# Performance work log

Hardware: AMD Instinct MI355X
Metric: run time of the kernel (lower is better)

The kernel has to match this reference:

```python
import jax, jax.numpy as jnp
import numpy as np
from jax import lax

DN = ('NCHW', 'OIHW', 'NCHW')


def setup_inputs() -> dict:
    key = jax.random.key(0)
    k_x, k0, k1, k2, k3 = jax.random.split(key, 5)
    return {
        'x': jax.random.normal(k_x, (16, 1, 256, 256), dtype=jnp.float32),
        'w0': jax.random.normal(k0, (16, 1, 25, 25), dtype=jnp.float32) * 0.05,
        'w1': jax.random.normal(k1, (16, 1, 49, 49), dtype=jnp.float32) * 0.02,
        'w2': jax.random.normal(k2, (16, 1, 97, 97), dtype=jnp.float32) * 0.01,
        'w3': jax.random.normal(k3, (16, 1, 193, 193), dtype=jnp.float32) * 0.005,
    }


def _energy(x, w, scale):
    # valid conv -> square -> global average pool, divided by scale. [B, 16]
    y = lax.conv_general_dilated(x, w, window_strides=(1, 1), padding='VALID',
                                 dimension_numbers=DN)
    return jnp.mean(y * y, axis=(2, 3)) / scale


def reference(x, w0, w1, w2, w3):
    feats = [
        _energy(x, w0, 1.0),
        _energy(x, w1, 2.0),
        _energy(x, w2, 4.0),
        _energy(x, w3, 8.0),
    ]
    y = jnp.stack(feats, axis=2)  # [B, 16, 4] == cat of squeezed [B,16,1] along dim 2
    y1, y2 = y[:, :8, :], y[:, 8:, :]  # split(8, dim=1)
    return y1 + y2  # [B, 8, 4]
```

## Files before the change

kernel.cpp:

```cpp
#include <hip/hip_runtime.h>
#include <hip/hip_bf16.h>

typedef __attribute__((ext_vector_type(8))) short short8v;
typedef __attribute__((ext_vector_type(4))) float f32x4;

#define IMG 256
#define NIMG 16
#define XB_ELEMS (NIMG * IMG * IMG)

#define WQ0 0u
#define WQ1 102400u
#define WQ2 503808u
#define WQ3 2093056u
#define WQEND 7624704u

#define BUFB 16384

__global__ void xconvert_kernel(const float* __restrict__ x,
                                __hip_bfloat16* __restrict__ xb) {
  int i = blockIdx.x * blockDim.x + threadIdx.x;
  if (i < XB_ELEMS) xb[i] = __float2bfloat16(x[i]);
}

__global__ void wpack_kernel(const float* __restrict__ w,
                             unsigned short* __restrict__ wq,
                             int K, int NSV, int total) {
  for (int idx = blockIdx.x * blockDim.x + threadIdx.x; idx < total;
       idx += gridDim.x * blockDim.x) {
    int e = idx & 7, lane = (idx >> 3) & 63, rest = idx >> 9;
    int sv = rest % NSV; rest /= NSV;
    int u = rest % K, sig = rest / K;
    int o = lane & 15;
    int v = sv * 32 + (lane >> 4) * 8 + e - sig;
    float val = (v >= 0 && v < K) ? w[(o * K + u) * K + v] : 0.0f;
    __hip_bfloat16 h = __float2bfloat16(val);
    wq[idx] = *(unsigned short*)&h;
  }
}

template <int GM, int NSV, int JBA>
__device__ __forceinline__ void kbody(int c, int rb0, int rb1, const char* bufc,
                                      const unsigned short* __restrict__ Wa,
                                      const unsigned short* __restrict__ Wb,
                                      int cbBase, int lr, f32x4 (&acc)[2][2][JBA]) {
#pragma unroll 1
  for (int rbL = rb0; rbL < rb1; ++rbL) {
    const int rowLoc = rbL + lr;
    const char* rbase = bufc + rowLoc * 512;
    const int u0i = 16 * c + rbL;
#pragma unroll
    for (int sv = 0; sv < NSV; ++sv) {
      short8v a_[JBA];
#pragma unroll
      for (int jb = 0; jb < JBA; ++jb) {
        int cb = cbBase + 16 * jb + 64 * sv;
        int addr = (cb & ~127) + ((((cb >> 4) ^ rowLoc) & 7) << 4);
        a_[jb] = *(const short8v*)(rbase + addr);
      }
      if (GM & 1) {
        const int wo = (u0i * NSV + sv) * 512;
        short8v ba = *(const short8v*)(Wa + wo);
        short8v bb = *(const short8v*)(Wb + wo);
#pragma unroll
        for (int jb = 0; jb < JBA; ++jb) {
          acc[0][0][jb] = __builtin_amdgcn_mfma_f32_16x16x32_bf16(a_[jb], ba, acc[0][0][jb], 0, 0, 0);
          acc[0][1][jb] = __builtin_amdgcn_mfma_f32_16x16x32_bf16(a_[jb], bb, acc[0][1][jb], 0, 0, 0);
        }
      }
      if (GM & 2) {
        const int wo = ((u0i - 16) * NSV + sv) * 512;
        short8v ba = *(const short8v*)(Wa + wo);
        short8v bb = *(const short8v*)(Wb + wo);
#pragma unroll
        for (int jb = 0; jb < JBA; ++jb) {
          acc[1][0][jb] = __builtin_amdgcn_mfma_f32_16x16x32_bf16(a_[jb], ba, acc[1][0][jb], 0, 0, 0);
          acc[1][1][jb] = __builtin_amdgcn_mfma_f32_16x16x32_bf16(a_[jb], bb, acc[1][1][jb], 0, 0, 0);
        }
      }
    }
  }
}

template <int KL, int KFULL, int NSV, int JBA, int WC, int HOUT, int SIDX>
__device__ __forceinline__ void conv_scale(const unsigned short* __restrict__ xb,
                                           const unsigned short* __restrict__ wq_s,
                                           float* __restrict__ E, char* lds,
                                           int n, int i0, int u0, int q) {
  constexpr int M16 = KL >> 4, R = KL & 15;
  constexpr int NCH = M16 + (R ? 2 : 1);
  constexpr unsigned SSTRIDE = (unsigned)KFULL * NSV * 512;

  const int wv = threadIdx.x >> 6, lane = threadIdx.x & 63;
  const int lr = lane & 15, lg = lane >> 4;
  const bool isProd = (WC < 8) && (wv >= WC);
  const unsigned short* Xn = xb + ((unsigned)n << 16);
  const int rowG0 = i0 + u0;

  const unsigned short* Wa = wq_s + (unsigned)(2 * q) * SSTRIDE +
                             (unsigned)(u0 * NSV) * 512 + lane * 8;
  const unsigned short* Wb = Wa + SSTRIDE;

  auto stage = [&](int cn) {
    char* dst = lds + (cn & 1) * BUFB;
    constexpr int NSTG = (WC < 8) ? (8 - WC) : 8;
    const int sid = (WC < 8) ? (wv - WC) : wv;
    constexpr int M = (16 + NSTG - 1) / NSTG;
#pragma unroll
    for (int k2 = 0; k2 < M; ++k2) {
      int ib = sid + NSTG * k2;
      if (ib >= 16) ib = 0;
      int P = ib * 1024 + lane * 16;
      int lrow = P >> 9;
      int slot = (P >> 4) & 31;
      int srcslot = (slot & ~7) | ((slot ^ lrow) & 7);
      int grow = rowG0 + cn * 16 + lrow;
      if (grow > 255) grow = 255;
      const unsigned short* gp = Xn + (grow << 8) + srcslot * 8;
      __builtin_amdgcn_global_load_lds(
          (const __attribute__((address_space(1))) unsigned int*)(const void*)gp,
          (__attribute__((address_space(3))) unsigned int*)(void*)(dst + P), 16, 0, 0);
    }
  };

  if (isProd) {
    stage(0);
    asm volatile("s_waitcnt vmcnt(0)" ::: "memory");
    __builtin_amdgcn_s_barrier();
    for (int c = 0; c < NCH; ++c) {
      if (c + 1 < NCH) {
        stage(c + 1);
        asm volatile("s_waitcnt vmcnt(0)" ::: "memory");
      }
      __builtin_amdgcn_s_barrier();
    }
    return;
  }

  f32x4 acc[2][2][JBA];
#pragma unroll
  for (int g = 0; g < 2; ++g)
#pragma unroll
    for (int sj = 0; sj < 2; ++sj)
#pragma unroll
      for (int jb = 0; jb < JBA; ++jb) acc[g][sj][jb] = (f32x4)(0.0f);

  const int t0 = wv * JBA;
  const int cbBase = 16 * t0 + 16 * lg;

  if (WC == 8) {
    stage(0);
    asm volatile("s_waitcnt vmcnt(0)" ::: "memory");
  }
  __builtin_amdgcn_s_barrier();

#define STEP_PRE(c)  if (WC == 8 && (c) + 1 < NCH) stage((c) + 1);
#define STEP_POST()  if (WC == 8) asm volatile("s_waitcnt vmcnt(0)" ::: "memory"); \
                     __builtin_amdgcn_s_barrier();

  {
    const char* bufc = lds;
    STEP_PRE(0)
    kbody<1, NSV, JBA>(0, 0, 16, bufc, Wa, Wb, cbBase, lr, acc);
    STEP_POST()
  }
#pragma unroll 1
  for (int c = 1; c < M16; ++c) {
    const char* bufc = lds + (c & 1) * BUFB;
    STEP_PRE(c)
    kbody<3, NSV, JBA>(c, 0, 16, bufc, Wa, Wb, cbBase, lr, acc);
    STEP_POST()
  }
  if (R > 0) {
    {
      const char* bufc = lds + (M16 & 1) * BUFB;
      STEP_PRE(M16)
      kbody<3, NSV, JBA>(M16, 0, R, bufc, Wa, Wb, cbBase, lr, acc);
      kbody<2, NSV, JBA>(M16, R, 16, bufc, Wa, Wb, cbBase, lr, acc);
      STEP_POST()
    }
    {
      const char* bufc = lds + ((M16 + 1) & 1) * BUFB;
      kbody<2, NSV, JBA>(M16 + 1, 0, R, bufc, Wa, Wb, cbBase, lr, acc);
      STEP_POST()
    }
  } else {
    const char* bufc = lds + (M16 & 1) * BUFB;
    kbody<2, NSV, JBA>(M16, 0, 16, bufc, Wa, Wb, cbBase, lr, acc);
    STEP_POST()
  }
#undef STEP_PRE
#undef STEP_POST

  float esum = 0.0f;
#pragma unroll
  for (int g = 0; g < 2; ++g)
#pragma unroll
    for (int sj = 0; sj < 2; ++sj)
#pragma unroll
      for (int jb = 0; jb < JBA; ++jb) {
        int j = 8 * (t0 + jb) + 2 * q + sj;
#pragma unroll
        for (int r2 = 0; r2 < 4; ++r2) {
          int i = i0 + 16 * g + 4 * lg + r2;
          float v = acc[g][sj][jb][r2];
          esum += (i < HOUT && j < HOUT) ? v * v : 0.0f;
        }
      }
  esum += __shfl_xor(esum, 16, 64);
  esum += __shfl_xor(esum, 32, 64);
  if (lg == 0) atomicAdd(&E[SIDX * 256 + n * 16 + lr], esum);
}

__global__ __launch_bounds__(512, 4) void conv_mfma_kernel(
    const unsigned short* __restrict__ xb, const unsigned short* __restrict__ wq,
    float* __restrict__ E) {
  __shared__ char lds[2 * BUFB];
  int b = blockIdx.x;
  if (b < 256) {
    int q = (b & 7) >> 1;
    int rest = ((b >> 3) << 1) | (b & 1);
    int ks = rest & 1, ig = (rest >> 1) & 1, n = rest >> 2;
    if (ks == 0) conv_scale<96, 193, 7, 2, 4, 64, 3>(xb, wq + WQ3, E, lds, n, ig * 32, 0, q);
    else         conv_scale<97, 193, 7, 2, 4, 64, 3>(xb, wq + WQ3, E, lds, n, ig * 32, 96, q);
  } else if (b < 896) {
    int bl = b - 256;
    int q = (bl & 7) >> 1;
    int rest = ((bl >> 3) << 1) | (bl & 1);
    int ks = rest & 1, r2 = rest >> 1;
    int ig = r2 % 5, n = r2 / 5;
    if (ks == 0) conv_scale<48, 97, 4, 4, 5, 160, 2>(xb, wq + WQ2, E, lds, n, ig * 32, 0, q);
    else         conv_scale<49, 97, 4, 4, 5, 160, 2>(xb, wq + WQ2, E, lds, n, ig * 32, 48, q);
  } else if (b < 1344) {
    int bl = b - 896;
    int q = (bl & 7) >> 1;
    int rest = ((bl >> 3) << 1) | (bl & 1);
    int ig = rest % 7, n = rest / 7;
    conv_scale<49, 49, 2, 4, 7, 208, 1>(xb, wq + WQ1, E, lds, n, ig * 32, 0, q);
  } else {
    int bl = b - 1344;
    int q = (bl & 7) >> 1;
    int rest = ((bl >> 3) << 1) | (bl & 1);
    int ig = rest & 7, n = rest >> 3;
    conv_scale<25, 25, 1, 4, 8, 232, 0>(xb, wq + WQ0, E, lds, n, ig * 32, 0, q);
  }
}

__global__ void finalize_kernel(const float* __restrict__ E, float* __restrict__ out) {
  int idx = threadIdx.x;
  if (idx >= 512) return;
  int s = idx & 3, c = (idx >> 2) & 7, n = idx >> 5;
  float denom;
  if (s == 0)      denom = 53824.0f;
  else if (s == 1) denom = 86528.0f;
  else if (s == 2) denom = 102400.0f;
  else             denom = 32768.0f;
  out[idx] = (E[s * 256 + n * 16 + c] + E[s * 256 + n * 16 + c + 8]) / denom;
}

extern "C" void kernel_launch(void* const* d_in, const int* in_sizes, int n_in,
                              void* d_out, int out_size, void* d_ws, size_t ws_size,
                              hipStream_t stream) {
  const float* x = (const float*)d_in[0];
  const float* w[4] = {(const float*)d_in[1], (const float*)d_in[2],
                       (const float*)d_in[3], (const float*)d_in[4]};
  static const int Ks[4] = {25, 49, 97, 193};
  static const int NSVs[4] = {1, 2, 4, 7};
  static const unsigned wOff[4] = {WQ0, WQ1, WQ2, WQ3};

  char* wsb = (char*)d_ws;
  float* E = (float*)wsb;
  __hip_bfloat16* xb = (__hip_bfloat16*)(wsb + 4096);
  unsigned short* wq = (unsigned short*)(wsb + 4096 + (size_t)XB_ELEMS * 2);

  hipMemsetAsync(E, 0, 1024 * sizeof(float), stream);
  xconvert_kernel<<<(XB_ELEMS + 255) / 256, 256, 0, stream>>>(x, xb);
  for (int s = 0; s < 4; ++s) {
    int total = 8 * Ks[s] * NSVs[s] * 512;
    wpack_kernel<<<2048, 256, 0, stream>>>(w[s], wq + wOff[s], Ks[s], NSVs[s], total);
  }
  conv_mfma_kernel<<<1856, 512, 0, stream>>>((const unsigned short*)xb, wq, E);
  finalize_kernel<<<1, 512, 0, stream>>>(E, (float*)d_out);
}
```

Baseline: 587.4 us.

## Fuse prep kernels, split smaller scales across column halves, raise MFMA priority

Folds the x conversion and the four weight-pack launches into one prep kernel, removing four launches. For the three smaller scales, each block now covers half the output columns (JBA 4 to 2, with a tile offset), which raises the grid from 1856 to 3456 blocks and cuts per-thread accumulator registers. MFMA compute sections are wrapped in s_setprio(1) so compute waves are favoured over staging waves. The cost is that each image row chunk gets staged into LDS twice for those scales, plus some extra block overhead.

```diff
diff --git a/kernel.cpp b/kernel.cpp
--- a/kernel.cpp
+++ b/kernel.cpp
@@ -16,26 +16,29 @@
 
 #define BUFB 16384
 
-__global__ void xconvert_kernel(const float* __restrict__ x,
-                                __hip_bfloat16* __restrict__ xb) {
-  int i = blockIdx.x * blockDim.x + threadIdx.x;
-  if (i < XB_ELEMS) xb[i] = __float2bfloat16(x[i]);
-}
-
-__global__ void wpack_kernel(const float* __restrict__ w,
-                             unsigned short* __restrict__ wq,
-                             int K, int NSV, int total) {
-  for (int idx = blockIdx.x * blockDim.x + threadIdx.x; idx < total;
-       idx += gridDim.x * blockDim.x) {
-    int e = idx & 7, lane = (idx >> 3) & 63, rest = idx >> 9;
-    int sv = rest % NSV; rest /= NSV;
-    int u = rest % K, sig = rest / K;
-    int o = lane & 15;
-    int v = sv * 32 + (lane >> 4) * 8 + e - sig;
-    float val = (v >= 0 && v < K) ? w[(o * K + u) * K + v] : 0.0f;
-    __hip_bfloat16 h = __float2bfloat16(val);
-    wq[idx] = *(unsigned short*)&h;
-  }
+__global__ void prep_kernel(const float* __restrict__ x,
+                            const float* __restrict__ w0, const float* __restrict__ w1,
+                            const float* __restrict__ w2, const float* __restrict__ w3,
+                            __hip_bfloat16* __restrict__ xb,
+                            unsigned short* __restrict__ wq) {
+  int idx = blockIdx.x * blockDim.x + threadIdx.x;
+  if (idx < XB_ELEMS) { xb[idx] = __float2bfloat16(x[idx]); return; }
+  int t = idx - XB_ELEMS;
+  if (t >= (int)WQEND) return;
+  const float* w; int K, NSV, base;
+  if (t < (int)WQ1)      { w = w0; K = 25;  NSV = 1; base = WQ0; }
+  else if (t < (int)WQ2) { w = w1; K = 49;  NSV = 2; base = WQ1; }
+  else if (t < (int)WQ3) { w = w2; K = 97;  NSV = 4; base = WQ2; }
+  else                   { w = w3; K = 193; NSV = 7; base = WQ3; }
+  int id2 = t - base;
+  int e = id2 & 7, lane = (id2 >> 3) & 63, rest = id2 >> 9;
+  int sv = rest % NSV; rest /= NSV;
+  int u = rest % K, sig = rest / K;
+  int o = lane & 15;
+  int v = sv * 32 + (lane >> 4) * 8 + e - sig;
+  float val = (v >= 0 && v < K) ? w[(o * K + u) * K + v] : 0.0f;
+  __hip_bfloat16 h = __float2bfloat16(val);
+  wq[t] = *(unsigned short*)&h;
 }
 
 template <int GM, int NSV, int JBA>
@@ -85,7 +88,7 @@
 __device__ __forceinline__ void conv_scale(const unsigned short* __restrict__ xb,
                                            const unsigned short* __restrict__ wq_s,
                                            float* __restrict__ E, char* lds,
-                                           int n, int i0, int u0, int q) {
+                                           int n, int i0, int u0, int q, int t0b) {
   constexpr int M16 = KL >> 4, R = KL & 15;
   constexpr int NCH = M16 + (R ? 2 : 1);
   constexpr unsigned SSTRIDE = (unsigned)KFULL * NSV * 512;
@@ -144,7 +147,7 @@
 #pragma unroll
       for (int jb = 0; jb < JBA; ++jb) acc[g][sj][jb] = (f32x4)(0.0f);
 
-  const int t0 = wv * JBA;
+  const int t0 = t0b + wv * JBA;
   const int cbBase = 16 * t0 + 16 * lg;
 
   if (WC == 8) {
@@ -160,32 +163,42 @@
   {
     const char* bufc = lds;
     STEP_PRE(0)
+    __builtin_amdgcn_s_setprio(1);
     kbody<1, NSV, JBA>(0, 0, 16, bufc, Wa, Wb, cbBase, lr, acc);
+    __builtin_amdgcn_s_setprio(0);
     STEP_POST()
   }
 #pragma unroll 1
   for (int c = 1; c < M16; ++c) {
     const char* bufc = lds + (c & 1) * BUFB;
     STEP_PRE(c)
+    __builtin_amdgcn_s_setprio(1);
     kbody<3, NSV, JBA>(c, 0, 16, bufc, Wa, Wb, cbBase, lr, acc);
+    __builtin_amdgcn_s_setprio(0);
     STEP_POST()
   }
   if (R > 0) {
     {
       const char* bufc = lds + (M16 & 1) * BUFB;
       STEP_PRE(M16)
+      __builtin_amdgcn_s_setprio(1);
       kbody<3, NSV, JBA>(M16, 0, R, bufc, Wa, Wb, cbBase, lr, acc);
       kbody<2, NSV, JBA>(M16, R, 16, bufc, Wa, Wb, cbBase, lr, acc);
+      __builtin_amdgcn_s_setprio(0);
       STEP_POST()
     }
     {
       const char* bufc = lds + ((M16 + 1) & 1) * BUFB;
+      __builtin_amdgcn_s_setprio(1);
       kbody<2, NSV, JBA>(M16 + 1, 0, R, bufc, Wa, Wb, cbBase, lr, acc);
+      __builtin_amdgcn_s_setprio(0);
       STEP_POST()
     }
   } else {
     const char* bufc = lds + (M16 & 1) * BUFB;
+    __builtin_amdgcn_s_setprio(1);
     kbody<2, NSV, JBA>(M16, 0, 16, bufc, Wa, Wb, cbBase, lr, acc);
+    __builtin_amdgcn_s_setprio(0);
     STEP_POST()
   }
 #undef STEP_PRE
@@ -220,28 +233,30 @@
     int q = (b & 7) >> 1;
     int rest = ((b >> 3) << 1) | (b & 1);
     int ks = rest & 1, ig = (rest >> 1) & 1, n = rest >> 2;
-    if (ks == 0) conv_scale<96, 193, 7, 2, 4, 64, 3>(xb, wq + WQ3, E, lds, n, ig * 32, 0, q);
-    else         conv_scale<97, 193, 7, 2, 4, 64, 3>(xb, wq + WQ3, E, lds, n, ig * 32, 96, q);
-  } else if (b < 896) {
+    if (ks == 0) conv_scale<96, 193, 7, 2, 4, 64, 3>(xb, wq + WQ3, E, lds, n, ig * 32, 0, q, 0);
+    else         conv_scale<97, 193, 7, 2, 4, 64, 3>(xb, wq + WQ3, E, lds, n, ig * 32, 96, q, 0);
+  } else if (b < 1536) {
     int bl = b - 256;
     int q = (bl & 7) >> 1;
     int rest = ((bl >> 3) << 1) | (bl & 1);
-    int ks = rest & 1, r2 = rest >> 1;
-    int ig = r2 % 5, n = r2 / 5;
-    if (ks == 0) conv_scale<48, 97, 4, 4, 5, 160, 2>(xb, wq + WQ2, E, lds, n, ig * 32, 0, q);
-    else         conv_scale<49, 97, 4, 4, 5, 160, 2>(xb, wq + WQ2, E, lds, n, ig * 32, 48, q);
-  } else if (b < 1344) {
-    int bl = b - 896;
+    int ks = rest & 1, ts = (rest >> 1) & 1, r = rest >> 2;
+    int ig = r % 5, n = r / 5;
+    if (ks == 0) conv_scale<48, 97, 4, 2, 5, 160, 2>(xb, wq + WQ2, E, lds, n, ig * 32, 0, q, ts * 10);
+    else         conv_scale<49, 97, 4, 2, 5, 160, 2>(xb, wq + WQ2, E, lds, n, ig * 32, 48, q, ts * 10);
+  } else if (b < 2432) {
+    int bl = b - 1536;
     int q = (bl & 7) >> 1;
     int rest = ((bl >> 3) << 1) | (bl & 1);
-    int ig = rest % 7, n = rest / 7;
-    conv_scale<49, 49, 2, 4, 7, 208, 1>(xb, wq + WQ1, E, lds, n, ig * 32, 0, q);
+    int ts = rest & 1, r = rest >> 1;
+    int ig = r % 7, n = r / 7;
+    conv_scale<49, 49, 2, 2, 7, 208, 1>(xb, wq + WQ1, E, lds, n, ig * 32, 0, q, ts * 14);
   } else {
-    int bl = b - 1344;
+    int bl = b - 2432;
     int q = (bl & 7) >> 1;
     int rest = ((bl >> 3) << 1) | (bl & 1);
-    int ig = rest & 7, n = rest >> 3;
-    conv_scale<25, 25, 1, 4, 8, 232, 0>(xb, wq + WQ0, E, lds, n, ig * 32, 0, q);
+    int ts = rest & 1, r = rest >> 1;
+    int ig = r & 7, n = r >> 3;
+    conv_scale<25, 25, 1, 2, 8, 232, 0>(xb, wq + WQ0, E, lds, n, ig * 32, 0, q, ts * 16);
   }
 }
 
@@ -261,11 +276,6 @@
                               void* d_out, int out_size, void* d_ws, size_t ws_size,
                               hipStream_t stream) {
   const float* x = (const float*)d_in[0];
-  const float* w[4] = {(const float*)d_in[1], (const float*)d_in[2],
-                       (const float*)d_in[3], (const float*)d_in[4]};
-  static const int Ks[4] = {25, 49, 97, 193};
-  static const int NSVs[4] = {1, 2, 4, 7};
-  static const unsigned wOff[4] = {WQ0, WQ1, WQ2, WQ3};
 
   char* wsb = (char*)d_ws;
   float* E = (float*)wsb;
@@ -273,11 +283,10 @@
   unsigned short* wq = (unsigned short*)(wsb + 4096 + (size_t)XB_ELEMS * 2);
 
   hipMemsetAsync(E, 0, 1024 * sizeof(float), stream);
-  xconvert_kernel<<<(XB_ELEMS + 255) / 256, 256, 0, stream>>>(x, xb);
-  for (int s = 0; s < 4; ++s) {
-    int total = 8 * Ks[s] * NSVs[s] * 512;
-    wpack_kernel<<<2048, 256, 0, stream>>>(w[s], wq + wOff[s], Ks[s], NSVs[s], total);
-  }
-  conv_mfma_kernel<<<1856, 512, 0, stream>>>((const unsigned short*)xb, wq, E);
+  int prepTotal = XB_ELEMS + (int)WQEND;
+  prep_kernel<<<(prepTotal + 255) / 256, 256, 0, stream>>>(
+      x, (const float*)d_in[1], (const float*)d_in[2], (const float*)d_in[3],
+      (const float*)d_in[4], xb, wq);
+  conv_mfma_kernel<<<3456, 512, 0, stream>>>((const unsigned short*)xb, wq, E);
   finalize_kernel<<<1, 512, 0, stream>>>(E, (float*)d_out);
 }
```

New measurement: 511.8 us. -12.9%, faster.
